# Optimization experiments

Hardware: AMD Instinct MI355X
Metric: run time of the kernel (lower is better)

## Reference

```python
import jax, jax.numpy as jnp
import numpy as np

B, T, I, H, O = 256, 500, 8, 1024, 8
ALPHA = 0.2
NOISE_STD = 0.05
BETA = 1.0
EXC_FRAC = 0.8   # fraction of excitatory presynaptic neurons
CONN_P = 0.3     # connectivity density of mask_wrec


def setup_inputs() -> dict:
    key = jax.random.key(0)
    ks = jax.random.split(key, 8)
    x = jax.random.normal(ks[0], (B, T, I), jnp.float32)
    noise = jax.random.normal(ks[1], (B, T, H), jnp.float32)
    wi = jax.random.normal(ks[2], (I, H), jnp.float32) / np.sqrt(I)
    wrec = jax.random.normal(ks[3], (H, H), jnp.float32) / np.sqrt(H)
    wout = jax.random.normal(ks[4], (H, O), jnp.float32) / np.sqrt(H)
    b = 0.1 * jax.random.normal(ks[5], (H, 1), jnp.float32)
    g = 0.3 * jax.random.uniform(ks[6], (H, 1), jnp.float32)
    h0 = jnp.ones((H,), jnp.float32)
    # Dale's law: sign set by presynaptic neuron j (effW[i,j] is weight j->i)
    ei = jnp.where(jnp.arange(H) < int(EXC_FRAC * H), 1.0, -1.0).astype(jnp.float32)
    refEI = jnp.tile(ei[None, :], (H, 1))  # [H,H]
    mwrec = (jax.random.uniform(ks[7], (H, H)) < CONN_P).astype(jnp.float32)
    return dict(x=x, noise=noise, wi=wi, wrec=wrec, wout=wout, b=b, g=g,
                h0=h0, refEI=refEI, mwrec=mwrec)


def _softplus_beta(v):
    # torch.nn.functional.softplus(v, beta) = (1/beta) * log(1 + exp(beta*v))
    return jax.nn.softplus(BETA * v) / BETA


def reference(x, noise, wi, wrec, wout, b, g, h0, refEI, mwrec):
    # EI-constrained effective weights (refEI entries are +/-1, so |refEI|-1 == 0)
    effW_ = jax.nn.relu(wrec * refEI) * refEI + (-wrec) * (jnp.abs(refEI) - 1.0)
    effW = effW_ * mwrec                    # [H,H]
    bT = b[:, 0]                            # [H]
    gr = jax.nn.relu(g[:, 0])               # [H]
    batch = x.shape[0]

    r0 = _softplus_beta(h0 + bT)            # [H]
    out0 = jnp.broadcast_to(r0 @ wout, (batch, wout.shape[1]))  # [B,O]

    inp_proj = jnp.einsum('bti,ih->bth', x, wi)  # [B,T,H]

    h_init = jnp.broadcast_to(h0, (batch, H))
    r_init = jnp.broadcast_to(r0, (batch, H))

    def step(carry, scanned):
        h, r = carry
        n_t, in_t = scanned  # [B,H] each
        h = h + NOISE_STD * n_t + ALPHA * (-h + (gr * r) @ effW.T + in_t)
        r = _softplus_beta(h + bT)
        return (h, r), r @ wout

    # steps i = 0 .. T-2 produce outputs 1 .. T-1
    noise_t = jnp.swapaxes(noise, 0, 1)[:-1]      # [T-1,B,H]
    inp_t = jnp.swapaxes(inp_proj, 0, 1)[:-1]     # [T-1,B,H]
    _, outs = jax.lax.scan(step, (h_init, r_init), (noise_t, inp_t))

    output = jnp.concatenate([out0[:, None, :], jnp.swapaxes(outs, 0, 1)], axis=1)
    return output  # [B,T,O]
```

## Files before the change

kernel.cpp:

```cpp
#include <hip/hip_runtime.h>

#define B_ 256
#define T_ 500
#define I_ 8
#define H_ 1024
#define O_ 8
#define NSTEP (T_ - 1)
#define EXC_N 819

typedef unsigned short u16;
typedef __attribute__((ext_vector_type(8))) short short8;
typedef __attribute__((ext_vector_type(4))) float f32x4;

__device__ __attribute__((aligned(16))) u16 g_rbuf[2 * B_ * H_];
__device__ unsigned int g_cnt[16 * 32];

__device__ __forceinline__ float bf2f(u16 u) {
    union { unsigned int i; float f; } v;
    v.i = ((unsigned int)u) << 16;
    return v.f;
}
__device__ __forceinline__ u16 f2bf(float f) {
    union { float f; unsigned int i; } v;
    v.f = f;
    unsigned int u = v.i;
    return (u16)((u + 0x7fffu + ((u >> 16) & 1u)) >> 16);
}
__device__ __forceinline__ float sp_(float v) {
    float e = __expf(-fabsf(v));
    return fmaxf(v, 0.0f) + __logf(1.0f + e);
}

__global__ void rnn_init() {
    g_cnt[threadIdx.x] = 0u;
    g_cnt[threadIdx.x + 256] = 0u;
}

__global__ void __launch_bounds__(256, 1)
rnn_persist(const float* __restrict__ x, const float* __restrict__ noise,
            const float* __restrict__ wi, const float* __restrict__ wrec,
            const float* __restrict__ wout, const float* __restrict__ bb,
            const float* __restrict__ gg, const float* __restrict__ h0,
            const float* __restrict__ mwrec, float* __restrict__ out)
{
    const int bid = blockIdx.x;
    const int grp = bid & 15;
    const int ntw = bid >> 4;
    const int jb  = ntw * 64;
    const int tid = threadIdx.x;
    const int w   = tid >> 6;
    const int l   = tid & 63;
    const int lm  = l & 15;
    const int lk  = l >> 4;
    const int kb  = w * 256;
    const int je  = jb + l;

    __shared__ float part[4 * 16 * 68];
    __shared__ float xbuf[16 * 8];
    __shared__ float outred[64];

    float wiv[8];
#pragma unroll
    for (int i = 0; i < 8; ++i) wiv[i] = wi[i * H_ + je];
    const float bTe = bb[je];
    float h[4];
    {
        float h0j = h0[je];
        h[0] = h[1] = h[2] = h[3] = h0j;
    }

    short8 Bf[8][4];
#pragma unroll
    for (int kf = 0; kf < 8; ++kf) {
#pragma unroll
        for (int n4 = 0; n4 < 4; ++n4) {
            const int jB = jb + n4 * 16 + lm;
            const int k0 = kb + kf * 32 + 8 * lk;
            short8 r;
#pragma unroll
            for (int i = 0; i < 8; ++i) {
                const int k = k0 + i;
                const float ei = (k < EXC_N) ? 1.0f : -1.0f;
                const float wf = wrec[jB * H_ + k];
                const float mf = mwrec[jB * H_ + k];
                const float gf = fmaxf(gg[k], 0.0f);
                const float e  = fmaxf(wf * ei, 0.0f) * ei * mf * gf;
                r[i] = (short)f2bf(e);
            }
            Bf[kf][n4] = r;
        }
    }

    float wo[64];
    if (ntw < O_) {
#pragma unroll
        for (int kf = 0; kf < 8; ++kf)
#pragma unroll
            for (int i = 0; i < 8; ++i) {
                const int k = kb + kf * 32 + 8 * lk + i;
                wo[kf * 8 + i] = wout[k * O_ + ntw];
            }
    }

    short8 Af[8];
#pragma unroll
    for (int kf = 0; kf < 8; ++kf) {
        const int k0 = kb + kf * 32 + 8 * lk;
        short8 a;
#pragma unroll
        for (int i = 0; i < 8; ++i)
            a[i] = (short)f2bf(sp_(h0[k0 + i] + bb[k0 + i]));
        Af[kf] = a;
    }

    float nprev[4];
#pragma unroll
    for (int q = 0; q < 4; ++q)
        nprev[q] = noise[(grp * 16 + w * 4 + q) * (T_ * H_) + je];
    float xp = 0.0f;
    if (tid < 128) xp = x[(grp * 16 + (tid >> 3)) * (T_ * I_) + (tid & 7)];

    unsigned int* myc = g_cnt + grp * 32;

    for (int t = 0; t < NSTEP; ++t) {
        if (tid < 128) xbuf[tid] = xp;

        f32x4 acc0 = {0,0,0,0}, acc1 = {0,0,0,0}, acc2 = {0,0,0,0}, acc3 = {0,0,0,0};
#pragma unroll
        for (int kf = 0; kf < 8; ++kf) {
            acc0 = __builtin_amdgcn_mfma_f32_16x16x32_bf16(Af[kf], Bf[kf][0], acc0, 0, 0, 0);
            acc1 = __builtin_amdgcn_mfma_f32_16x16x32_bf16(Af[kf], Bf[kf][1], acc1, 0, 0, 0);
            acc2 = __builtin_amdgcn_mfma_f32_16x16x32_bf16(Af[kf], Bf[kf][2], acc2, 0, 0, 0);
            acc3 = __builtin_amdgcn_mfma_f32_16x16x32_bf16(Af[kf], Bf[kf][3], acc3, 0, 0, 0);
        }
#pragma unroll
        for (int reg = 0; reg < 4; ++reg) {
            const int m = 4 * lk + reg;
            part[(w * 16 + m) * 68 +  0 + lm] = acc0[reg];
            part[(w * 16 + m) * 68 + 16 + lm] = acc1[reg];
            part[(w * 16 + m) * 68 + 32 + lm] = acc2[reg];
            part[(w * 16 + m) * 68 + 48 + lm] = acc3[reg];
        }
        __syncthreads();

        u16 rsto[4];
#pragma unroll
        for (int q = 0; q < 4; ++q) {
            const int m = w * 4 + q;
            float D = part[(0 * 16 + m) * 68 + l] + part[(1 * 16 + m) * 68 + l]
                    + part[(2 * 16 + m) * 68 + l] + part[(3 * 16 + m) * 68 + l];
            float inp = 0.0f;
#pragma unroll
            for (int i = 0; i < 8; ++i) inp = fmaf(xbuf[m * 8 + i], wiv[i], inp);
            float hn = h[q] + 0.05f * nprev[q] + 0.2f * (-h[q] + D + inp);
            hn = fminf(fmaxf(hn, -64.0f), 64.0f);
            h[q] = hn;
            rsto[q] = f2bf(sp_(hn + bTe));
        }
        {
            unsigned int* rb32 = (unsigned int*)(g_rbuf + ((t + 1) & 1) * (B_ * H_)
                                                 + (grp * 16) * H_);
#pragma unroll
            for (int q = 0; q < 4; ++q) {
                unsigned int mine = (unsigned int)rsto[q];
                unsigned int nb   = (unsigned int)__shfl_xor((int)mine, 1, 64);
                if ((l & 1) == 0) {
                    unsigned int packed = (mine & 0xffffu) | (nb << 16);
                    __hip_atomic_store(rb32 + (((w * 4 + q) * H_ + je) >> 1), packed,
                                       __ATOMIC_RELAXED, __HIP_MEMORY_SCOPE_AGENT);
                }
            }
        }

        asm volatile("s_waitcnt vmcnt(0)" ::: "memory");
        __syncthreads();
        if (tid == 0)
            __hip_atomic_fetch_add(myc, 1u, __ATOMIC_RELAXED, __HIP_MEMORY_SCOPE_AGENT);

#pragma unroll
        for (int q = 0; q < 4; ++q)
            nprev[q] = noise[(grp * 16 + w * 4 + q) * (T_ * H_) + (t + 1) * H_ + je];
        if (tid < 128 && t + 1 < NSTEP)
            xp = x[(grp * 16 + (tid >> 3)) * (T_ * I_) + (t + 1) * I_ + (tid & 7)];

        if (ntw < O_) {
            float po = 0.0f;
#pragma unroll
            for (int kf = 0; kf < 8; ++kf) {
                const short8 a = Af[kf];
#pragma unroll
                for (int i = 0; i < 8; ++i)
                    po = fmaf(bf2f((u16)a[i]), wo[kf * 8 + i], po);
            }
            po += __shfl_xor(po, 16, 64);
            po += __shfl_xor(po, 32, 64);
            if (l < 16) outred[w * 16 + l] = po;
            __syncthreads();
            if (tid < 16) {
                float s = outred[tid] + outred[16 + tid] + outred[32 + tid] + outred[48 + tid];
                out[(grp * 16 + tid) * (T_ * O_) + t * O_ + ntw] = s;
            }
        }

        if (tid == 0) {
            const unsigned int tgt = 16u * (unsigned)(t + 1);
            while (__hip_atomic_load(myc, __ATOMIC_RELAXED, __HIP_MEMORY_SCOPE_AGENT) < tgt) { }
        }
        __syncthreads();

        {
            u16* rbl = g_rbuf + ((t + 1) & 1) * (B_ * H_) + (grp * 16 + lm) * H_ + kb;
#pragma unroll
            for (int kf = 0; kf < 8; ++kf) {
                unsigned long long* p = (unsigned long long*)(rbl + kf * 32 + 8 * lk);
                unsigned long long d0 = __hip_atomic_load(p + 0, __ATOMIC_RELAXED,
                                                          __HIP_MEMORY_SCOPE_AGENT);
                unsigned long long d1 = __hip_atomic_load(p + 1, __ATOMIC_RELAXED,
                                                          __HIP_MEMORY_SCOPE_AGENT);
                union { unsigned long long q[2]; short8 s; } cv;
                cv.q[0] = d0; cv.q[1] = d1;
                Af[kf] = cv.s;
            }
        }
    }

    if (ntw < O_) {
        float po = 0.0f;
#pragma unroll
        for (int kf = 0; kf < 8; ++kf) {
            const short8 a = Af[kf];
#pragma unroll
            for (int i = 0; i < 8; ++i)
                po = fmaf(bf2f((u16)a[i]), wo[kf * 8 + i], po);
        }
        po += __shfl_xor(po, 16, 64);
        po += __shfl_xor(po, 32, 64);
        if (l < 16) outred[w * 16 + l] = po;
        __syncthreads();
        if (tid < 16) {
            float s = outred[tid] + outred[16 + tid] + outred[32 + tid] + outred[48 + tid];
            out[(grp * 16 + tid) * (T_ * O_) + (T_ - 1) * O_ + ntw] = s;
        }
    }
}

extern "C" void kernel_launch(void* const* d_in, const int* in_sizes, int n_in,
                              void* d_out, int out_size, void* d_ws, size_t ws_size,
                              hipStream_t stream) {
    (void)in_sizes; (void)n_in; (void)out_size; (void)d_ws; (void)ws_size;
    const float* x     = (const float*)d_in[0];
    const float* noise = (const float*)d_in[1];
    const float* wi    = (const float*)d_in[2];
    const float* wrec  = (const float*)d_in[3];
    const float* wout  = (const float*)d_in[4];
    const float* bb    = (const float*)d_in[5];
    const float* gg    = (const float*)d_in[6];
    const float* h0    = (const float*)d_in[7];
    const float* mwrec = (const float*)d_in[9];
    float* out = (float*)d_out;

    rnn_init<<<dim3(1), dim3(256), 0, stream>>>();
    rnn_persist<<<dim3(256), dim3(256), 0, stream>>>(
        x, noise, wi, wrec, wout, bb, gg, h0, mwrec, out);
}
```

Before: 2.800 ms.

## Replace group counter barrier with per-block flags and partial-wait reads

Swaps the shared atomic counter barrier for per-block step flags. Each wave polls only the producer flags it needs, with its 16 lanes checking 16 blocks, before reading its slice of the recurrent state. A lazy write-side check guards the double buffer against overwrite only when some producer lagged. The output, noise and x global loads/stores move after the rbuf reads so they don't sit in front of the wait, cutting barrier latency and contention on one counter. The risk is that ordering now rests on relaxed atomics and the write-side guard.

```diff
diff --git a/kernel.cpp b/kernel.cpp
--- a/kernel.cpp
+++ b/kernel.cpp
@@ -13,7 +13,7 @@
 typedef __attribute__((ext_vector_type(4))) float f32x4;
 
 __device__ __attribute__((aligned(16))) u16 g_rbuf[2 * B_ * H_];
-__device__ unsigned int g_cnt[16 * 32];
+__device__ __attribute__((aligned(128))) unsigned int g_flag[16 * 32];
 
 __device__ __forceinline__ float bf2f(u16 u) {
     union { unsigned int i; float f; } v;
@@ -32,8 +32,8 @@
 }
 
 __global__ void rnn_init() {
-    g_cnt[threadIdx.x] = 0u;
-    g_cnt[threadIdx.x + 256] = 0u;
+    g_flag[threadIdx.x] = 0u;
+    g_flag[threadIdx.x + 256] = 0u;
 }
 
 __global__ void __launch_bounds__(256, 1)
@@ -120,7 +120,8 @@
     float xp = 0.0f;
     if (tid < 128) xp = x[(grp * 16 + (tid >> 3)) * (T_ * I_) + (tid & 7)];
 
-    unsigned int* myc = g_cnt + grp * 32;
+    unsigned int* flg = g_flag + grp * 32;
+    bool all16_ok = true;
 
     for (int t = 0; t < NSTEP; ++t) {
         if (tid < 128) xbuf[tid] = xp;
@@ -157,6 +158,15 @@
             h[q] = hn;
             rsto[q] = f2bf(sp_(hn + bTe));
         }
+
+        if (!all16_ok) {
+            unsigned int f;
+            do {
+                f = __hip_atomic_load(flg + lm, __ATOMIC_RELAXED, __HIP_MEMORY_SCOPE_AGENT);
+            } while (!__all((int)(f >= (unsigned int)t)));
+        }
+        asm volatile("" ::: "memory");
+
         {
             unsigned int* rb32 = (unsigned int*)(g_rbuf + ((t + 1) & 1) * (B_ * H_)
                                                  + (grp * 16) * H_);
@@ -172,17 +182,7 @@
             }
         }
 
-        asm volatile("s_waitcnt vmcnt(0)" ::: "memory");
-        __syncthreads();
-        if (tid == 0)
-            __hip_atomic_fetch_add(myc, 1u, __ATOMIC_RELAXED, __HIP_MEMORY_SCOPE_AGENT);
-
-#pragma unroll
-        for (int q = 0; q < 4; ++q)
-            nprev[q] = noise[(grp * 16 + w * 4 + q) * (T_ * H_) + (t + 1) * H_ + je];
-        if (tid < 128 && t + 1 < NSTEP)
-            xp = x[(grp * 16 + (tid >> 3)) * (T_ * I_) + (t + 1) * I_ + (tid & 7)];
-
+        float outval = 0.0f;
         if (ntw < O_) {
             float po = 0.0f;
 #pragma unroll
@@ -196,17 +196,26 @@
             po += __shfl_xor(po, 32, 64);
             if (l < 16) outred[w * 16 + l] = po;
             __syncthreads();
-            if (tid < 16) {
-                float s = outred[tid] + outred[16 + tid] + outred[32 + tid] + outred[48 + tid];
-                out[(grp * 16 + tid) * (T_ * O_) + t * O_ + ntw] = s;
-            }
-        }
-
-        if (tid == 0) {
-            const unsigned int tgt = 16u * (unsigned)(t + 1);
-            while (__hip_atomic_load(myc, __ATOMIC_RELAXED, __HIP_MEMORY_SCOPE_AGENT) < tgt) { }
-        }
+            if (tid < 16)
+                outval = outred[tid] + outred[16 + tid] + outred[32 + tid] + outred[48 + tid];
+        }
+
+        asm volatile("s_waitcnt vmcnt(0)" ::: "memory");
         __syncthreads();
+        if (tid == 0)
+            __hip_atomic_store(flg + ntw, (unsigned int)(t + 1),
+                               __ATOMIC_RELAXED, __HIP_MEMORY_SCOPE_AGENT);
+
+        unsigned long long rdy;
+        {
+            const unsigned int tgt = (unsigned int)(t + 1);
+            do {
+                unsigned int f = __hip_atomic_load(flg + lm, __ATOMIC_RELAXED,
+                                                   __HIP_MEMORY_SCOPE_AGENT);
+                rdy = __ballot((int)(f >= tgt));
+            } while (((rdy >> (4 * w)) & 0xFull) != 0xFull);
+        }
+        all16_ok = (~rdy == 0ull);
 
         {
             u16* rbl = g_rbuf + ((t + 1) & 1) * (B_ * H_) + (grp * 16 + lm) * H_ + kb;
@@ -222,6 +231,14 @@
                 Af[kf] = cv.s;
             }
         }
+
+        if (ntw < O_ && tid < 16)
+            out[(grp * 16 + tid) * (T_ * O_) + t * O_ + ntw] = outval;
+#pragma unroll
+        for (int q = 0; q < 4; ++q)
+            nprev[q] = noise[(grp * 16 + w * 4 + q) * (T_ * H_) + (t + 1) * H_ + je];
+        if (tid < 128 && t + 1 < NSTEP)
+            xp = x[(grp * 16 + (tid >> 3)) * (T_ * I_) + (t + 1) * I_ + (tid & 7)];
     }
 
     if (ntw < O_) {
```

Result: slower. 3.366 ms (+20.2%).

## Replace counter barrier with sign-bit flag polling embedded in bf16 state

Applied to the files above, without the earlier changes.

Removes the per-group atomic counter barrier (vmcnt wait, syncthreads, atomic add, spin by thread 0, syncthreads). Each consumer now spins directly on the packed bf16 r values, using the sign bit (always zero for softplus outputs) as a phase flag that alternates every two steps. Shared scratch buffers are double-buffered so the removed barrier is not needed for WAR safety, and the init kernel seeds the flag bits. This cuts synchronisation latency per step, but it relies on a relaxed-store ordering and adds repeated 16-byte polling traffic.

```diff
diff --git a/kernel.cpp b/kernel.cpp
--- a/kernel.cpp
+++ b/kernel.cpp
@@ -11,9 +11,9 @@
 typedef unsigned short u16;
 typedef __attribute__((ext_vector_type(8))) short short8;
 typedef __attribute__((ext_vector_type(4))) float f32x4;
+typedef __attribute__((ext_vector_type(4))) unsigned int u32x4;
 
 __device__ __attribute__((aligned(16))) u16 g_rbuf[2 * B_ * H_];
-__device__ unsigned int g_cnt[16 * 32];
 
 __device__ __forceinline__ float bf2f(u16 u) {
     union { unsigned int i; float f; } v;
@@ -32,8 +32,10 @@
 }
 
 __global__ void rnn_init() {
-    g_cnt[threadIdx.x] = 0u;
-    g_cnt[threadIdx.x + 256] = 0u;
+    const unsigned int idx = blockIdx.x * 256 + threadIdx.x;
+    u32x4* p = (u32x4*)g_rbuf;
+    const unsigned int z = 0u, s = 0x80008000u;
+    p[idx] = (idx < 32768u) ? (u32x4){z, z, z, z} : (u32x4){s, s, s, s};
 }
 
 __global__ void __launch_bounds__(256, 1)
@@ -55,8 +57,8 @@
     const int kb  = w * 256;
     const int je  = jb + l;
 
-    __shared__ float part[4 * 16 * 68];
-    __shared__ float xbuf[16 * 8];
+    __shared__ float part[2][4 * 16 * 68];
+    __shared__ float xbuf[2][16 * 8];
     __shared__ float outred[64];
 
     float wiv[8];
@@ -120,10 +122,9 @@
     float xp = 0.0f;
     if (tid < 128) xp = x[(grp * 16 + (tid >> 3)) * (T_ * I_) + (tid & 7)];
 
-    unsigned int* myc = g_cnt + grp * 32;
-
     for (int t = 0; t < NSTEP; ++t) {
-        if (tid < 128) xbuf[tid] = xp;
+        const int pp = t & 1;
+        if (tid < 128) xbuf[pp][tid] = xp;
 
         f32x4 acc0 = {0,0,0,0}, acc1 = {0,0,0,0}, acc2 = {0,0,0,0}, acc3 = {0,0,0,0};
 #pragma unroll
@@ -136,26 +137,27 @@
 #pragma unroll
         for (int reg = 0; reg < 4; ++reg) {
             const int m = 4 * lk + reg;
-            part[(w * 16 + m) * 68 +  0 + lm] = acc0[reg];
-            part[(w * 16 + m) * 68 + 16 + lm] = acc1[reg];
-            part[(w * 16 + m) * 68 + 32 + lm] = acc2[reg];
-            part[(w * 16 + m) * 68 + 48 + lm] = acc3[reg];
+            part[pp][(w * 16 + m) * 68 +  0 + lm] = acc0[reg];
+            part[pp][(w * 16 + m) * 68 + 16 + lm] = acc1[reg];
+            part[pp][(w * 16 + m) * 68 + 32 + lm] = acc2[reg];
+            part[pp][(w * 16 + m) * 68 + 48 + lm] = acc3[reg];
         }
         __syncthreads();
 
+        const u16 sbit = (u16)(((((unsigned)(t + 1)) >> 1) & 1u) << 15);
         u16 rsto[4];
 #pragma unroll
         for (int q = 0; q < 4; ++q) {
             const int m = w * 4 + q;
-            float D = part[(0 * 16 + m) * 68 + l] + part[(1 * 16 + m) * 68 + l]
-                    + part[(2 * 16 + m) * 68 + l] + part[(3 * 16 + m) * 68 + l];
+            float D = part[pp][(0 * 16 + m) * 68 + l] + part[pp][(1 * 16 + m) * 68 + l]
+                    + part[pp][(2 * 16 + m) * 68 + l] + part[pp][(3 * 16 + m) * 68 + l];
             float inp = 0.0f;
 #pragma unroll
-            for (int i = 0; i < 8; ++i) inp = fmaf(xbuf[m * 8 + i], wiv[i], inp);
+            for (int i = 0; i < 8; ++i) inp = fmaf(xbuf[pp][m * 8 + i], wiv[i], inp);
             float hn = h[q] + 0.05f * nprev[q] + 0.2f * (-h[q] + D + inp);
             hn = fminf(fmaxf(hn, -64.0f), 64.0f);
             h[q] = hn;
-            rsto[q] = f2bf(sp_(hn + bTe));
+            rsto[q] = (u16)(f2bf(sp_(hn + bTe)) | sbit);
         }
         {
             unsigned int* rb32 = (unsigned int*)(g_rbuf + ((t + 1) & 1) * (B_ * H_)
@@ -172,17 +174,13 @@
             }
         }
 
-        asm volatile("s_waitcnt vmcnt(0)" ::: "memory");
-        __syncthreads();
-        if (tid == 0)
-            __hip_atomic_fetch_add(myc, 1u, __ATOMIC_RELAXED, __HIP_MEMORY_SCOPE_AGENT);
-
 #pragma unroll
         for (int q = 0; q < 4; ++q)
             nprev[q] = noise[(grp * 16 + w * 4 + q) * (T_ * H_) + (t + 1) * H_ + je];
         if (tid < 128 && t + 1 < NSTEP)
             xp = x[(grp * 16 + (tid >> 3)) * (T_ * I_) + (t + 1) * I_ + (tid & 7)];
 
+        float outval = 0.0f;
         if (ntw < O_) {
             float po = 0.0f;
 #pragma unroll
@@ -196,34 +194,45 @@
             po += __shfl_xor(po, 32, 64);
             if (l < 16) outred[w * 16 + l] = po;
             __syncthreads();
-            if (tid < 16) {
-                float s = outred[tid] + outred[16 + tid] + outred[32 + tid] + outred[48 + tid];
-                out[(grp * 16 + tid) * (T_ * O_) + t * O_ + ntw] = s;
-            }
-        }
-
-        if (tid == 0) {
-            const unsigned int tgt = 16u * (unsigned)(t + 1);
-            while (__hip_atomic_load(myc, __ATOMIC_RELAXED, __HIP_MEMORY_SCOPE_AGENT) < tgt) { }
-        }
-        __syncthreads();
+            if (tid < 16)
+                outval = outred[tid] + outred[16 + tid] + outred[32 + tid] + outred[48 + tid];
+        }
 
         {
+            const unsigned long long SM = 0x8000800080008000ull;
+            const unsigned long long SE = (((unsigned)(t + 1) >> 1) & 1u) ? SM : 0ull;
             u16* rbl = g_rbuf + ((t + 1) & 1) * (B_ * H_) + (grp * 16 + lm) * H_ + kb;
+            unsigned long long d0[8], d1[8];
+            int ok;
+            do {
+#pragma unroll
+                for (int kf = 0; kf < 8; ++kf) {
+                    unsigned long long* p = (unsigned long long*)(rbl + kf * 32 + 8 * lk);
+                    d0[kf] = __hip_atomic_load(p + 0, __ATOMIC_RELAXED,
+                                               __HIP_MEMORY_SCOPE_AGENT);
+                    d1[kf] = __hip_atomic_load(p + 1, __ATOMIC_RELAXED,
+                                               __HIP_MEMORY_SCOPE_AGENT);
+                }
+                unsigned long long bad = 0ull;
+#pragma unroll
+                for (int kf = 0; kf < 8; ++kf)
+                    bad |= ((d0[kf] ^ SE) & SM) | ((d1[kf] ^ SE) & SM);
+                ok = (bad == 0ull);
+            } while (!ok);
 #pragma unroll
             for (int kf = 0; kf < 8; ++kf) {
-                unsigned long long* p = (unsigned long long*)(rbl + kf * 32 + 8 * lk);
-                unsigned long long d0 = __hip_atomic_load(p + 0, __ATOMIC_RELAXED,
-                                                          __HIP_MEMORY_SCOPE_AGENT);
-                unsigned long long d1 = __hip_atomic_load(p + 1, __ATOMIC_RELAXED,
-                                                          __HIP_MEMORY_SCOPE_AGENT);
                 union { unsigned long long q[2]; short8 s; } cv;
-                cv.q[0] = d0; cv.q[1] = d1;
+                cv.q[0] = d0[kf] & ~SM;
+                cv.q[1] = d1[kf] & ~SM;
                 Af[kf] = cv.s;
             }
         }
-    }
-
+
+        if (ntw < O_ && tid < 16)
+            out[(grp * 16 + tid) * (T_ * O_) + t * O_ + ntw] = outval;
+    }
+
+    __syncthreads();
     if (ntw < O_) {
         float po = 0.0f;
 #pragma unroll
@@ -259,7 +268,7 @@
     const float* mwrec = (const float*)d_in[9];
     float* out = (float*)d_out;
 
-    rnn_init<<<dim3(1), dim3(256), 0, stream>>>();
+    rnn_init<<<dim3(256), dim3(256), 0, stream>>>();
     rnn_persist<<<dim3(256), dim3(256), 0, stream>>>(
         x, noise, wi, wrec, wout, bb, gg, h0, mwrec, out);
 }
```

Result: no change. 2.767 ms (-1.2%).
